# Kernel optimization log

Hardware: AMD Instinct MI355X
Metric: run time of the kernel (lower is better)

Reference implementation:

```python
import jax, jax.numpy as jnp
import numpy as np
from jax import lax

# pywt db5 analysis filter bank (frozen buffers in the torch module)
DEC_LO = np.array([0.003335725285001549, -0.012580751999015526, -0.006241490213011705,
                   0.07757149384006515, -0.03224486958502952, -0.24229488706619015,
                   0.13842814590110342, 0.7243085284385744, 0.6038292697974729,
                   0.160102397974125], dtype=np.float32)
DEC_HI = np.array([-0.160102397974125, 0.6038292697974729, -0.7243085284385744,
                   0.13842814590110342, 0.24229488706619015, -0.03224486958502952,
                   -0.07757149384006515, -0.006241490213011705, 0.012580751999015526,
                   0.003335725285001549], dtype=np.float32)
NUM_LEVELS = 8  # min(round(log2(131072)), max_level=8)


def _conv1d(x, w, padding, lhs_dilation=(1,), groups=1):
    # x: [N, C, L], w: [O, I, K]; cross-correlation, matching torch F.conv1d
    return lax.conv_general_dilated(
        x, w, window_strides=(1,), padding=[padding], lhs_dilation=lhs_dilation,
        dimension_numbers=("NCH", "OIH", "NCH"), feature_group_count=groups)


def setup_inputs() -> dict:
    key = jax.random.key(0)
    k1, k2 = jax.random.split(key)
    x = jax.random.normal(k1, (128, 131072), dtype=jnp.float32)
    # small scale keeps the 8-level synthesis cascade numerically tame
    idwt_filters = jax.random.normal(k2, (128, 8, 2, 32), dtype=jnp.float32) * 0.05
    return {"x": x, "idwt_filters": idwt_filters}


def reference(x, idwt_filters):
    # x: [B, T]; idwt_filters: [B, levels, 2, kw] with kw even
    B, T = x.shape
    w_lo = jnp.asarray(DEC_LO).reshape(1, 1, -1)
    w_hi = jnp.asarray(DEC_HI).reshape(1, 1, -1)
    pad = DEC_LO.shape[0] // 2  # 5 -> conv output length L+1 for kernel 10

    # --- analysis DWT (frozen db5 filters), lengths: T/2^l + 1 per band ---
    lo = x[:, None, :]                       # [B,1,T]
    his = []
    for _ in range(NUM_LEVELS):
        y_lo = _conv1d(lo, w_lo, (pad, pad))
        y_hi = _conv1d(lo, w_hi, (pad, pad))
        lo = y_lo[:, :, ::2]
        his.append(y_hi[:, :, ::2])          # [B,1,T/2^l+1]

    # --- synthesis IDWT with predicted per-example filters (groups=B) ---
    kw = idwt_filters.shape[-1]
    p = kw // 2 - 1
    prev = jnp.transpose(lo, (1, 0, 2))      # [1,B,n]: batch as channels
    for i in range(NUM_LEVELS - 1, -1, -1):
        rec_lo = idwt_filters[:, i, 0, :][:, None, :]   # [B,1,kw]
        rec_hi = idwt_filters[:, i, 1, :][:, None, :]
        hi = jnp.transpose(his[i], (1, 0, 2))           # [1,B,n]
        # lhs_dilation=2 == zero-stuffing even indices; asym pad (p, p+1)
        # reproduces torch's trailing zero at index 2n-1; out length = 2n-1
        y_lo = _conv1d(prev, rec_lo, (p, p + 1), lhs_dilation=(2,), groups=B)
        y_hi = _conv1d(hi, rec_hi, (p, p + 1), lhs_dilation=(2,), groups=B)
        prev = y_lo + y_hi
    return prev[0, :, :-1]                   # [B, T]
```

## Files before the change

### kernel.cpp

```cpp
#include <hip/hip_runtime.h>


static __constant__ float c_dec_lo[10] = {
    0.003335725285001549f, -0.012580751999015526f, -0.006241490213011705f,
    0.07757149384006515f, -0.03224486958502952f, -0.24229488706619015f,
    0.13842814590110342f, 0.7243085284385744f, 0.6038292697974729f,
    0.160102397974125f};
static __constant__ float c_dec_hi[10] = {
    -0.160102397974125f, 0.6038292697974729f, -0.7243085284385744f,
    0.13842814590110342f, 0.24229488706619015f, -0.03224486958502952f,
    -0.07757149384006515f, -0.006241490213011705f, 0.012580751999015526f,
    0.003335725285001549f};

__device__ inline float4 ldz4(const float* __restrict__ row, int j, int L) {
  if (j >= 0 && j + 3 < L) return *reinterpret_cast<const float4*>(row + j);
  float4 r;
  r.x = (j + 0 >= 0 && j + 0 < L) ? row[j + 0] : 0.f;
  r.y = (j + 1 >= 0 && j + 1 < L) ? row[j + 1] : 0.f;
  r.z = (j + 2 >= 0 && j + 2 < L) ? row[j + 2] : 0.f;
  r.w = (j + 3 >= 0 && j + 3 < L) ? row[j + 3] : 0.f;
  return r;
}

__device__ inline void load20(const float* src, int base, float* v) {
#pragma unroll
  for (int q = 0; q < 5; ++q) {
    const float4 t = *reinterpret_cast<const float4*>(src + base + 4 * q);
    v[4 * q + 0] = t.x; v[4 * q + 1] = t.y;
    v[4 * q + 2] = t.z; v[4 * q + 3] = t.w;
  }
}

__device__ inline void load20z(const float* __restrict__ src, int base, int L,
                               float* v) {
#pragma unroll
  for (int q = 0; q < 5; ++q) {
    const float4 t = ldz4(src, base + 4 * q, L);
    v[4 * q + 0] = t.x; v[4 * q + 1] = t.y;
    v[4 * q + 2] = t.z; v[4 * q + 3] = t.w;
  }
}

__device__ inline void fir10x2(const float* v, float* lo, float* hv) {
#pragma unroll
  for (int i = 0; i < 4; ++i) {
    float a = 0.f, h = 0.f;
#pragma unroll
    for (int k = 0; k < 10; ++k) {
      const float xx = v[2 * i + 3 + k];
      a += xx * c_dec_lo[k];
      h += xx * c_dec_hi[k];
    }
    lo[i] = a; hv[i] = h;
  }
}

__device__ inline void store_pad(float* S, int idx, const float* lo, int vlo,
                                 int vhi) {
  if (idx >= vlo && idx + 3 < vhi) {
    *reinterpret_cast<float4*>(S + idx) =
        make_float4(lo[0], lo[1], lo[2], lo[3]);
  } else {
#pragma unroll
    for (int i = 0; i < 4; ++i)
      S[idx + i] = (idx + i >= vlo && idx + i < vhi) ? lo[i] : 0.f;
  }
}

__device__ inline void store_hi(float* hg, int A, int idx, const float* hv,
                                int es, int ee) {
  if (idx >= es && idx + 3 < ee) {
    *reinterpret_cast<float4*>(hg + A + idx) =
        make_float4(hv[0], hv[1], hv[2], hv[3]);
  } else {
#pragma unroll
    for (int i = 0; i < 4; ++i)
      if (idx + i >= es && idx + i < ee) hg[A + idx + i] = hv[i];
  }
}

__device__ inline void st4(float* dst, const float* a) {
  *reinterpret_cast<float4*>(dst) = make_float4(a[0], a[1], a[2], a[3]);
}

__global__ __launch_bounds__(256) void fwd03(
    const float* __restrict__ x, float* __restrict__ hi0,
    float* __restrict__ hi1, float* __restrict__ hi2,
    float* __restrict__ hi3, float* __restrict__ lo3) {
  const int b = blockIdx.y;
  const int bx = blockIdx.x;
  const int b3 = bx * 512;
  __shared__ float S0[4180];
  __shared__ float S1[2084];
  const int tid = threadIdx.x;
  const bool fast = (bx >= 1) && (bx <= 14);
  const float* xr = x + (size_t)b * 131072;
  float* h0 = hi0 + (size_t)b * 65540;
  float* h1 = hi1 + (size_t)b * 32772;
  float* h2 = hi2 + (size_t)b * 16388;
  float* h3 = hi3 + (size_t)b * 8196;
  float* l3 = lo3 + (size_t)b * 8196;
  const int A0 = 8 * b3 - 56, A1 = 4 * b3 - 24, A2 = 2 * b3 - 8;
  const int xoff = 2 * A0 - 8;

  if (fast) {
    for (int idx = 4 * tid; idx < 4180; idx += 1024) {
      float v[20]; load20(xr, 2 * idx + xoff, v);
      float lo[4], hv[4]; fir10x2(v, lo, hv);
      st4(S0 + idx, lo);
      if (idx >= 56 && idx < 4152) st4(h0 + A0 + idx, hv);
    }
    __syncthreads();
    for (int idx = 4 * tid; idx < 2084; idx += 1024) {
      float v[20]; load20(S0, 2 * idx, v);
      float lo[4], hv[4]; fir10x2(v, lo, hv);
      st4(S1 + idx, lo);
      if (idx >= 24 && idx < 2072) st4(h1 + A1 + idx, hv);
    }
    __syncthreads();
    for (int idx = 4 * tid; idx < 1036; idx += 1024) {
      float v[20]; load20(S1, 2 * idx, v);
      float lo[4], hv[4]; fir10x2(v, lo, hv);
      st4(S0 + idx, lo);
      if (idx >= 8 && idx < 1032) st4(h2 + A2 + idx, hv);
    }
    __syncthreads();
    for (int idx = 4 * tid; idx < 512; idx += 1024) {
      float v[20]; load20(S0, 2 * idx, v);
      float lo[4], hv[4]; fir10x2(v, lo, hv);
      st4(l3 + b3 + idx, lo);
      st4(h3 + b3 + idx, hv);
    }
  } else {
    {
      const int vlo = -A0, vhi = 65537 - A0;
      const int ee = min(4152, vhi);
      for (int idx = 4 * tid; idx < 4180; idx += 1024) {
        float v[20]; load20z(xr, 2 * idx + xoff, 131072, v);
        float lo[4], hv[4]; fir10x2(v, lo, hv);
        store_pad(S0, idx, lo, vlo, vhi);
        store_hi(h0, A0, idx, hv, 56, ee);
      }
    }
    __syncthreads();
    {
      const int vlo = -A1, vhi = 32769 - A1;
      const int ee = min(2072, vhi);
      for (int idx = 4 * tid; idx < 2084; idx += 1024) {
        float v[20]; load20(S0, 2 * idx, v);
        float lo[4], hv[4]; fir10x2(v, lo, hv);
        store_pad(S1, idx, lo, vlo, vhi);
        store_hi(h1, A1, idx, hv, 24, ee);
      }
    }
    __syncthreads();
    {
      const int vlo = -A2, vhi = 16385 - A2;
      const int ee = min(1032, vhi);
      for (int idx = 4 * tid; idx < 1036; idx += 1024) {
        float v[20]; load20(S1, 2 * idx, v);
        float lo[4], hv[4]; fir10x2(v, lo, hv);
        store_pad(S0, idx, lo, vlo, vhi);
        store_hi(h2, A2, idx, hv, 8, ee);
      }
    }
    __syncthreads();
    {
      const int ne3 = min(512, 8193 - b3);
      for (int idx = 4 * tid; idx < 512; idx += 1024) {
        float v[20]; load20(S0, 2 * idx, v);
        float lo[4], hv[4]; fir10x2(v, lo, hv);
        store_hi(l3, b3, idx, lo, 0, ne3);
        store_hi(h3, b3, idx, hv, 0, ne3);
      }
    }
  }
}

__device__ inline void inv_accum(const float* p, const float* h,
                                 const float4* wpk, float* acc) {
#pragma unroll
  for (int i = 0; i < 8; ++i) acc[i] = 0.f;
#pragma unroll
  for (int m = 0; m < 16; ++m) {
    const float4 w = wpk[m];
#pragma unroll
    for (int e = 0; e < 4; ++e) {
      const float pe = p[e + 1 + m], he = h[e + 1 + m];
      acc[2 * e + 0] += pe * w.y + he * w.w;
      acc[2 * e + 1] += pe * w.x + he * w.z;
    }
  }
}

__device__ inline void inv_store_pad(float* S, int o, const float* acc,
                                     int vlo, int vhi) {
  if (o >= vlo && o + 7 < vhi) {
    st4(S + o, acc);
    st4(S + o + 4, acc + 4);
  } else {
#pragma unroll
    for (int i = 0; i < 8; ++i)
      S[o + i] = (o + i >= vlo && o + i < vhi) ? acc[i] : 0.f;
  }
}

template <bool FAST>
__device__ inline void inv_stage_g(const float* __restrict__ pg,
                                   const float* __restrict__ hig, int Dp,
                                   int P0, float* Sout, int NOUT, int Aout,
                                   int lenOut, const float4* wpk, int tid) {
  const int vlo = -Aout, vhi = lenOut - Aout;
  for (int o = 8 * tid; o < NOUT; o += 2048) {
    const int uh = o >> 1;
    float p[20], h[20];
    if (FAST) {
      load20(pg, P0 + uh, p);
      load20(hig, P0 + uh, h);
    } else {
      load20z(pg, P0 + uh, Dp, p);
      load20z(hig, P0 + uh, Dp, h);
    }
    float acc[8];
    inv_accum(p, h, wpk, acc);
    if (FAST) {
      st4(Sout + o, acc);
      st4(Sout + o + 4, acc + 4);
    } else {
      inv_store_pad(Sout, o, acc, vlo, vhi);
    }
  }
}

template <bool FAST>
__device__ inline void inv_stage_l(const float* Sprev, int reloff,
                                   const float* __restrict__ hig, int Dhi,
                                   int U0, float* Sout, int NOUT, int Aout,
                                   int lenOut, const float4* wpk, int tid) {
  const int vlo = -Aout, vhi = lenOut - Aout;
  for (int o = 8 * tid; o < NOUT; o += 2048) {
    const int uh = o >> 1;
    float p[20], h[20];
    load20(Sprev, uh + reloff, p);
    if (FAST) load20(hig, U0 + uh, h);
    else load20z(hig, U0 + uh, Dhi, h);
    float acc[8];
    inv_accum(p, h, wpk, acc);
    if (FAST) {
      st4(Sout + o, acc);
      st4(Sout + o + 4, acc + 4);
    } else {
      inv_store_pad(Sout, o, acc, vlo, vhi);
    }
  }
}

template <bool FAST>
__device__ inline void inv_stage_o(const float* Sprev,
                                   const float* __restrict__ hig, int Dhi,
                                   int U0, float* __restrict__ og,
                                   const float4* wpk, int tid) {
  for (int o = 8 * tid; o < 8192; o += 2048) {
    const int uh = o >> 1;
    float p[20], h[20];
    load20(Sprev, uh, p);
    if (FAST) load20(hig, U0 + uh, h);
    else load20z(hig, U0 + uh, Dhi, h);
    float acc[8];
    inv_accum(p, h, wpk, acc);
    st4(og + o, acc);
    st4(og + o + 4, acc + 4);
  }
}

__global__ __launch_bounds__(256) void inv03(
    const float* __restrict__ prev3, const float* __restrict__ hi3,
    const float* __restrict__ hi2, const float* __restrict__ hi1,
    const float* __restrict__ hi0, const float* __restrict__ filt,
    float* __restrict__ out) {
  const int c = blockIdx.y;
  const int bx = blockIdx.x;
  const int t0b = bx * 8192;
  __shared__ float X[4112];
  __shared__ float Y[2080];
  __shared__ float4 wp[64];
  const int tid = threadIdx.x;
  if (tid < 64) {
    const int lvl = tid >> 4, m = tid & 15;
    const float* f = filt + ((size_t)c * 8 + (3 - lvl)) * 64;
    wp[tid] = make_float4(f[2 * m], f[2 * m + 1], f[32 + 2 * m],
                          f[32 + 2 * m + 1]);
  }
  __syncthreads();
  const bool fast = (bx >= 1) && (bx <= 14);
  const float* p3 = prev3 + (size_t)c * 8196;
  const float* h3 = hi3 + (size_t)c * 8196;
  const float* h2 = hi2 + (size_t)c * 16388;
  const float* h1 = hi1 + (size_t)c * 32772;
  const float* h0 = hi0 + (size_t)c * 65540;
  float* og = out + (size_t)c * 131072 + t0b;

  if (fast) {
    inv_stage_g<true>(p3, h3, 8193, t0b / 16 - 16, X, 1056, t0b / 8 - 16,
                      16385, wp, tid);
    __syncthreads();
    inv_stage_l<true>(X, 0, h2, 16385, t0b / 8 - 16, Y, 2080, t0b / 4 - 16,
                      32769, wp + 16, tid);
    __syncthreads();
    inv_stage_l<true>(Y, 4, h1, 32769, t0b / 4 - 12, X, 4112, t0b / 2 - 8,
                      65537, wp + 32, tid);
    __syncthreads();
    inv_stage_o<true>(X, h0, 65537, t0b / 2 - 8, og, wp + 48, tid);
  } else {
    inv_stage_g<false>(p3, h3, 8193, t0b / 16 - 16, X, 1056, t0b / 8 - 16,
                       16385, wp, tid);
    __syncthreads();
    inv_stage_l<false>(X, 0, h2, 16385, t0b / 8 - 16, Y, 2080, t0b / 4 - 16,
                       32769, wp + 16, tid);
    __syncthreads();
    inv_stage_l<false>(Y, 4, h1, 32769, t0b / 4 - 12, X, 4112, t0b / 2 - 8,
                       65537, wp + 32, tid);
    __syncthreads();
    inv_stage_o<false>(X, h0, 65537, t0b / 2 - 8, og, wp + 48, tid);
  }
}

__device__ inline void fwd_tail_level(const float* __restrict__ in,
                                      float* __restrict__ outp, int L, int D,
                                      float* __restrict__ hirow, int tid) {
  for (int d0 = 4 * tid; d0 < D; d0 += 2048) {
    const int jb = 2 * d0 - 8;
    float v[20];
    const bool interior = (jb >= 0) && (jb + 19 < L) && (d0 + 3 < D);
    if (interior) {
      load20(in, jb, v);
    } else {
#pragma unroll
      for (int q = 0; q < 20; ++q) {
        const int j = jb + q;
        v[q] = (j >= 0 && j < L) ? in[j] : 0.f;
      }
    }
    float lo[4], hv[4];
    fir10x2(v, lo, hv);
    if (interior) {
      st4(outp + d0, lo);
      st4(hirow + d0, hv);
    } else {
#pragma unroll
      for (int i = 0; i < 4; ++i)
        if (d0 + i < D) { outp[d0 + i] = lo[i]; hirow[d0 + i] = hv[i]; }
    }
  }
}

__device__ inline void inv_tail_level(const float* __restrict__ pin,
                                      float* __restrict__ pout, int L,
                                      const float* __restrict__ hirow,
                                      const float* __restrict__ filt, int c,
                                      int level, int tid, float4* wpack) {
  __syncthreads();
  if (tid < 16) {
    const float* f = filt + ((size_t)c * 8 + level) * 64;
    wpack[tid] = make_float4(f[2 * tid], f[2 * tid + 1], f[32 + 2 * tid],
                             f[32 + 2 * tid + 1]);
  }
  __syncthreads();
  const int Tout = 2 * L - 1;
  for (int t0 = 8 * tid; t0 < Tout; t0 += 4096) {
    const int U = t0 / 2 - 8;
    float p[20], h[20];
    if (U >= 0 && U + 19 < L) {
      load20(pin, U, p);
      load20(hirow, U, h);
    } else {
#pragma unroll
      for (int q = 0; q < 20; ++q) {
        const int j = U + q;
        p[q] = (j >= 0 && j < L) ? pin[j] : 0.f;
        h[q] = (j >= 0 && j < L) ? hirow[j] : 0.f;
      }
    }
    float acc[8];
    inv_accum(p, h, wpack, acc);
    if (t0 + 7 < Tout) {
      st4(pout + t0, acc);
      st4(pout + t0 + 4, acc + 4);
    } else {
#pragma unroll
      for (int i = 0; i < 8; ++i)
        if (t0 + i < Tout) pout[t0 + i] = acc[i];
    }
  }
}

__global__ __launch_bounds__(512) void mid_fused(
    const float* __restrict__ lo3, const float* __restrict__ filt,
    float* __restrict__ prev3out) {
  const int b = blockIdx.x;
  __shared__ float A[8200];
  __shared__ float Bb[4104];
  __shared__ float H4[4100];
  __shared__ float H5[2052];
  __shared__ float H6[1028];
  __shared__ float H7[516];
  __shared__ float4 wpack[16];
  const int tid = threadIdx.x;
  const float* row = lo3 + (size_t)b * 8196;
  for (int j4 = tid; j4 < 2048; j4 += 512)
    *reinterpret_cast<float4*>(A + 4 * j4) =
        *reinterpret_cast<const float4*>(row + 4 * j4);
  if (tid == 0) A[8192] = row[8192];
  __syncthreads();
  fwd_tail_level(A, Bb, 8193, 4097, H4, tid);
  __syncthreads();
  fwd_tail_level(Bb, A, 4097, 2049, H5, tid);
  __syncthreads();
  fwd_tail_level(A, Bb, 2049, 1025, H6, tid);
  __syncthreads();
  fwd_tail_level(Bb, A, 1025, 513, H7, tid);
  inv_tail_level(A, Bb, 513, H7, filt, b, 7, tid, wpack);
  inv_tail_level(Bb, A, 1025, H6, filt, b, 6, tid, wpack);
  inv_tail_level(A, Bb, 2049, H5, filt, b, 5, tid, wpack);
  inv_tail_level(Bb, prev3out + (size_t)b * 8196, 4097, H4, filt, b, 4, tid,
                 wpack);
}

extern "C" void kernel_launch(void* const* d_in, const int* in_sizes, int n_in,
                              void* d_out, int out_size, void* d_ws,
                              size_t ws_size, hipStream_t stream) {
  const float* x = (const float*)d_in[0];
  const float* filt = (const float*)d_in[1];
  float* out = (float*)d_out;
  float* ws = (float*)d_ws;

  const int B = 128;
  float* lo3buf = ws;
  float* prev3buf = lo3buf + (size_t)B * 8196;
  float* hi0 = prev3buf + (size_t)B * 8196;
  float* hi1 = hi0 + (size_t)B * 65540;
  float* hi2 = hi1 + (size_t)B * 32772;
  float* hi3 = hi2 + (size_t)B * 16388;

  hipLaunchKernelGGL(fwd03, dim3(17, B), dim3(256), 0, stream, x, hi0, hi1,
                     hi2, hi3, lo3buf);
  hipLaunchKernelGGL(mid_fused, dim3(B), dim3(512), 0, stream, lo3buf, filt,
                     prev3buf);
  hipLaunchKernelGGL(inv03, dim3(16, B), dim3(256), 0, stream, prev3buf, hi3,
                     hi2, hi1, hi0, filt, out);
}
```

Measured before the change: 149.7 us.

## Split fused inverse cascade into per-level global-memory kernels

Replaces the single inverse kernel that chained the last four synthesis levels through shared memory with four launches of a generic per-level kernel. Each level writes its reconstruction to new workspace buffers, and each thread computes 16 outputs from 24 loaded coefficients. This removes the halo recomputation and block-wide barriers of the fused tiling. In exchange it adds global-memory round trips for the intermediates and three more kernel launches.

```diff
diff --git a/kernel.cpp b/kernel.cpp
--- a/kernel.cpp
+++ b/kernel.cpp
@@ -193,135 +193,66 @@
   }
 }
 
-__device__ inline void inv_store_pad(float* S, int o, const float* acc,
-                                     int vlo, int vhi) {
-  if (o >= vlo && o + 7 < vhi) {
-    st4(S + o, acc);
-    st4(S + o + 4, acc + 4);
-  } else {
-#pragma unroll
-    for (int i = 0; i < 8; ++i)
-      S[o + i] = (o + i >= vlo && o + i < vhi) ? acc[i] : 0.f;
-  }
-}
-
-template <bool FAST>
-__device__ inline void inv_stage_g(const float* __restrict__ pg,
-                                   const float* __restrict__ hig, int Dp,
-                                   int P0, float* Sout, int NOUT, int Aout,
-                                   int lenOut, const float4* wpk, int tid) {
-  const int vlo = -Aout, vhi = lenOut - Aout;
-  for (int o = 8 * tid; o < NOUT; o += 2048) {
-    const int uh = o >> 1;
-    float p[20], h[20];
-    if (FAST) {
-      load20(pg, P0 + uh, p);
-      load20(hig, P0 + uh, h);
-    } else {
-      load20z(pg, P0 + uh, Dp, p);
-      load20z(hig, P0 + uh, Dp, h);
-    }
-    float acc[8];
-    inv_accum(p, h, wpk, acc);
-    if (FAST) {
-      st4(Sout + o, acc);
-      st4(Sout + o + 4, acc + 4);
-    } else {
-      inv_store_pad(Sout, o, acc, vlo, vhi);
-    }
-  }
-}
-
-template <bool FAST>
-__device__ inline void inv_stage_l(const float* Sprev, int reloff,
-                                   const float* __restrict__ hig, int Dhi,
-                                   int U0, float* Sout, int NOUT, int Aout,
-                                   int lenOut, const float4* wpk, int tid) {
-  const int vlo = -Aout, vhi = lenOut - Aout;
-  for (int o = 8 * tid; o < NOUT; o += 2048) {
-    const int uh = o >> 1;
-    float p[20], h[20];
-    load20(Sprev, uh + reloff, p);
-    if (FAST) load20(hig, U0 + uh, h);
-    else load20z(hig, U0 + uh, Dhi, h);
-    float acc[8];
-    inv_accum(p, h, wpk, acc);
-    if (FAST) {
-      st4(Sout + o, acc);
-      st4(Sout + o + 4, acc + 4);
-    } else {
-      inv_store_pad(Sout, o, acc, vlo, vhi);
-    }
-  }
-}
-
-template <bool FAST>
-__device__ inline void inv_stage_o(const float* Sprev,
-                                   const float* __restrict__ hig, int Dhi,
-                                   int U0, float* __restrict__ og,
-                                   const float4* wpk, int tid) {
-  for (int o = 8 * tid; o < 8192; o += 2048) {
-    const int uh = o >> 1;
-    float p[20], h[20];
-    load20(Sprev, uh, p);
-    if (FAST) load20(hig, U0 + uh, h);
-    else load20z(hig, U0 + uh, Dhi, h);
-    float acc[8];
-    inv_accum(p, h, wpk, acc);
-    st4(og + o, acc);
-    st4(og + o + 4, acc + 4);
-  }
-}
-
-__global__ __launch_bounds__(256) void inv03(
-    const float* __restrict__ prev3, const float* __restrict__ hi3,
-    const float* __restrict__ hi2, const float* __restrict__ hi1,
-    const float* __restrict__ hi0, const float* __restrict__ filt,
-    float* __restrict__ out) {
+__global__ __launch_bounds__(256) void inv_big(
+    const float* __restrict__ prev, const float* __restrict__ hicoef,
+    const float* __restrict__ filt, int level, int L, int sIn, int Tout,
+    int sOut, float* __restrict__ out) {
   const int c = blockIdx.y;
-  const int bx = blockIdx.x;
-  const int t0b = bx * 8192;
-  __shared__ float X[4112];
-  __shared__ float Y[2080];
-  __shared__ float4 wp[64];
+  __shared__ float4 wpack[16];
   const int tid = threadIdx.x;
-  if (tid < 64) {
-    const int lvl = tid >> 4, m = tid & 15;
-    const float* f = filt + ((size_t)c * 8 + (3 - lvl)) * 64;
-    wp[tid] = make_float4(f[2 * m], f[2 * m + 1], f[32 + 2 * m],
-                          f[32 + 2 * m + 1]);
-  }
-  __syncthreads();
-  const bool fast = (bx >= 1) && (bx <= 14);
-  const float* p3 = prev3 + (size_t)c * 8196;
-  const float* h3 = hi3 + (size_t)c * 8196;
-  const float* h2 = hi2 + (size_t)c * 16388;
-  const float* h1 = hi1 + (size_t)c * 32772;
-  const float* h0 = hi0 + (size_t)c * 65540;
-  float* og = out + (size_t)c * 131072 + t0b;
-
-  if (fast) {
-    inv_stage_g<true>(p3, h3, 8193, t0b / 16 - 16, X, 1056, t0b / 8 - 16,
-                      16385, wp, tid);
-    __syncthreads();
-    inv_stage_l<true>(X, 0, h2, 16385, t0b / 8 - 16, Y, 2080, t0b / 4 - 16,
-                      32769, wp + 16, tid);
-    __syncthreads();
-    inv_stage_l<true>(Y, 4, h1, 32769, t0b / 4 - 12, X, 4112, t0b / 2 - 8,
-                      65537, wp + 32, tid);
-    __syncthreads();
-    inv_stage_o<true>(X, h0, 65537, t0b / 2 - 8, og, wp + 48, tid);
-  } else {
-    inv_stage_g<false>(p3, h3, 8193, t0b / 16 - 16, X, 1056, t0b / 8 - 16,
-                       16385, wp, tid);
-    __syncthreads();
-    inv_stage_l<false>(X, 0, h2, 16385, t0b / 8 - 16, Y, 2080, t0b / 4 - 16,
-                       32769, wp + 16, tid);
-    __syncthreads();
-    inv_stage_l<false>(Y, 4, h1, 32769, t0b / 4 - 12, X, 4112, t0b / 2 - 8,
-                       65537, wp + 32, tid);
-    __syncthreads();
-    inv_stage_o<false>(X, h0, 65537, t0b / 2 - 8, og, wp + 48, tid);
+  if (tid < 16) {
+    const float* f = filt + ((size_t)c * 8 + level) * 64;
+    wpack[tid] = make_float4(f[2 * tid], f[2 * tid + 1],
+                             f[32 + 2 * tid], f[32 + 2 * tid + 1]);
+  }
+  __syncthreads();
+  const int g = blockIdx.x * 256 + tid;
+  const int t0 = 16 * g;
+  if (t0 >= Tout) return;
+  const int U = 8 * g - 8;
+  const float* prow = prev + (size_t)c * sIn;
+  const float* hrow = hicoef + (size_t)c * sIn;
+  float p[24], h[24];
+  const bool interior = (U >= 0) && (U + 23 < L) && (t0 + 15 < Tout);
+  if (interior) {
+#pragma unroll
+    for (int q = 0; q < 6; ++q) {
+      float4 a = *reinterpret_cast<const float4*>(prow + U + 4 * q);
+      p[4 * q + 0] = a.x; p[4 * q + 1] = a.y; p[4 * q + 2] = a.z; p[4 * q + 3] = a.w;
+      float4 bb = *reinterpret_cast<const float4*>(hrow + U + 4 * q);
+      h[4 * q + 0] = bb.x; h[4 * q + 1] = bb.y; h[4 * q + 2] = bb.z; h[4 * q + 3] = bb.w;
+    }
+  } else {
+#pragma unroll
+    for (int q = 0; q < 24; ++q) {
+      const int j = U + q;
+      p[q] = (j >= 0 && j < L) ? prow[j] : 0.f;
+      h[q] = (j >= 0 && j < L) ? hrow[j] : 0.f;
+    }
+  }
+  float acc[16];
+#pragma unroll
+  for (int i = 0; i < 16; ++i) acc[i] = 0.f;
+#pragma unroll
+  for (int m = 0; m < 16; ++m) {
+    const float4 w = wpack[m];
+#pragma unroll
+    for (int e = 0; e < 8; ++e) {
+      const float pv = p[e + 1 + m], hv = h[e + 1 + m];
+      acc[2 * e + 0] += pv * w.y + hv * w.w;
+      acc[2 * e + 1] += pv * w.x + hv * w.z;
+    }
+  }
+  float* orow = out + (size_t)c * sOut;
+  if (interior) {
+#pragma unroll
+    for (int q = 0; q < 4; ++q)
+      *reinterpret_cast<float4*>(orow + t0 + 4 * q) =
+          make_float4(acc[4 * q], acc[4 * q + 1], acc[4 * q + 2], acc[4 * q + 3]);
+  } else {
+#pragma unroll
+    for (int i = 0; i < 16; ++i)
+      if (t0 + i < Tout) orow[t0 + i] = acc[i];
   }
 }
 
@@ -441,11 +372,24 @@
   float* hi1 = hi0 + (size_t)B * 65540;
   float* hi2 = hi1 + (size_t)B * 32772;
   float* hi3 = hi2 + (size_t)B * 16388;
+  float* prev2buf = hi3 + (size_t)B * 8196;
+  float* prev1buf = prev2buf + (size_t)B * 16388;
+  float* prev0buf = prev1buf + (size_t)B * 32772;
 
   hipLaunchKernelGGL(fwd03, dim3(17, B), dim3(256), 0, stream, x, hi0, hi1,
                      hi2, hi3, lo3buf);
   hipLaunchKernelGGL(mid_fused, dim3(B), dim3(512), 0, stream, lo3buf, filt,
                      prev3buf);
-  hipLaunchKernelGGL(inv03, dim3(16, B), dim3(256), 0, stream, prev3buf, hi3,
-                     hi2, hi1, hi0, filt, out);
-}
+
+  auto launch_inv = [&](const float* prev, const float* hv, int level, int L,
+                        int sIn, int Tout, int sOut, float* dst) {
+    const int tpr = (Tout + 15) / 16;
+    dim3 grid((tpr + 255) / 256, B);
+    hipLaunchKernelGGL(inv_big, grid, dim3(256), 0, stream, prev, hv, filt,
+                       level, L, sIn, Tout, sOut, dst);
+  };
+  launch_inv(prev3buf, hi3, 3, 8193, 8196, 16385, 16388, prev2buf);
+  launch_inv(prev2buf, hi2, 2, 16385, 16388, 32769, 32772, prev1buf);
+  launch_inv(prev1buf, hi1, 1, 32769, 32772, 65537, 65540, prev0buf);
+  launch_inv(prev0buf, hi0, 0, 65537, 65540, 131072, 131072, out);
+}
```

After: 135.7 us. 9.4% less time.
